# Kernel optimization log

Measured on AMD Instinct MI355X. Metric: run time of the kernel, lower is better.

## Reference

```python
import jax, jax.numpy as jnp
import numpy as np


def _conv1x1(w, x):
    # w: [out, in], x: [B, in, H, W] -> [B, out, H, W]
    return jnp.einsum('oc,bchw->bohw', w, x)


def _maxpool2(x):
    # 2x2 max pool, stride 2. x: [B, C, H, W] -> [B, C, H//2, W//2]
    B, C, H, W = x.shape
    return x.reshape(B, C, H // 2, 2, W // 2, 2).max(axis=(3, 5))


def setup_inputs() -> dict:
    key = jax.random.key(0)
    ks = jax.random.split(key, 5)
    B, C, H, W = 8, 256, 64, 64
    div = 8
    x = jax.random.normal(ks[0], (B, C, H, W), dtype=jnp.float32)
    wq = jax.random.normal(ks[1], (C // div, C), dtype=jnp.float32) * (C ** -0.5)
    wk = jax.random.normal(ks[2], (C // div, C), dtype=jnp.float32) * (C ** -0.5)
    wv = jax.random.normal(ks[3], (C // 2, C), dtype=jnp.float32) * (C ** -0.5)
    wo = jax.random.normal(ks[4], (C, C // 2), dtype=jnp.float32) * ((C // 2) ** -0.5)
    gamma = jnp.float32(0.5)  # nonzero so attention branch contributes
    return {"x": x, "wq": wq, "wk": wk, "wv": wv, "wo": wo, "gamma": gamma}


def reference(x, wq, wk, wv, wo, gamma):
    B, C, H, W = x.shape
    HW = H * W
    # query: [B, HW, Cq]
    q = _conv1x1(wq, x).reshape(B, -1, HW).transpose(0, 2, 1)
    # key: maxpool -> [B, Cq, HW//4]
    k = _maxpool2(_conv1x1(wk, x)).reshape(B, -1, HW // 4)
    # value: maxpool -> [B, C//2, HW//4]
    v = _maxpool2(_conv1x1(wv, x)).reshape(B, -1, HW // 4)
    scores = jnp.einsum('bnc,bcm->bnm', q, k)          # [B, HW, HW//4]
    attn = jax.nn.softmax(scores, axis=2)
    ctx = jnp.einsum('bcm,bnm->bcn', v, attn)          # [B, C//2, HW]
    ctx = ctx.reshape(B, C // 2, H, W)
    out = gamma * _conv1x1(wo, ctx) + x
    return out
```

## Files before the change

kernel.cpp:

```cpp
#include <hip/hip_runtime.h>
#include <hip/hip_bf16.h>

#define BB  8
#define CC  256
#define HW  4096
#define CQ  32
#define CV  128
#define MP  1024

#define XT_OFF  0
#define Y_OFF   4194304
#define KT_OFF  (Y_OFF + 3145728)
#define VP_OFF  (KT_OFF + 131072)
#define CT_OFF  (VP_OFF + 524288)
#define P0_OFF  CT_OFF
#define P1_OFF  XT_OFF
#define ML_OFF  (XT_OFF + 2097152)

typedef __attribute__((ext_vector_type(8))) short bf16x8;
typedef __attribute__((ext_vector_type(4))) short short4v;
typedef __attribute__((ext_vector_type(4))) float f32x4;

__device__ __forceinline__ short f2b(float f) {
    unsigned u = __float_as_uint(f);
    u += 0x7fffu + ((u >> 16) & 1u);
    return (short)(u >> 16);
}
__device__ __forceinline__ float b2f(short s) {
    return __uint_as_float(((unsigned)(unsigned short)s) << 16);
}

__global__ __launch_bounds__(256) void k_xt(
    const float* __restrict__ x, short* __restrict__ xt)
{
    __shared__ float t[64][65];
    const int bid = blockIdx.x;
    const int nt = bid & 63;
    const int ct = (bid >> 6) & 3;
    const int b  = bid >> 8;
    const int c0 = ct * 64, n0 = nt * 64;
    const int tid = threadIdx.x;

    const int col = tid & 63, wrow = (tid >> 6) * 16;
    #pragma unroll
    for (int i = 0; i < 16; ++i) {
        int r = wrow + i;
        t[r][col] = x[((long)(b * CC + c0 + r)) * HW + n0 + col];
    }
    __syncthreads();

    const int n = tid >> 2, cb = (tid & 3) * 16;
    short buf[16];
    #pragma unroll
    for (int j = 0; j < 16; ++j) buf[j] = f2b(t[cb + j][n]);
    short* dst = &xt[((long)(b * HW + n0 + n)) * CC + c0 + cb];
    *(int4*)dst = *(int4*)&buf[0];
    *(int4*)(dst + 8) = *(int4*)&buf[8];
}

__global__ __launch_bounds__(256) void k_qkv(
    const float* __restrict__ wq, const float* __restrict__ wk,
    const float* __restrict__ wv, const short* __restrict__ xt,
    short* __restrict__ y)
{
    __shared__ short w_lds[96 * 264];
    __shared__ short x_lds[256 * 40];
    const int bid = blockIdx.x;
    const int oc = bid & 1;
    const int nt = (bid >> 1) & 15;
    const int b  = bid >> 5;
    const int o0 = oc * 96, n0 = nt * 256;
    const int tid = threadIdx.x;
    const int lane = tid & 63;
    const int wvid = tid >> 6;
    const int l15 = lane & 15, g = lane >> 4;

    for (int it = 0; it < 24; ++it) {
        int idx = tid + it * 256;
        int ol = idx >> 6, cq = (idx & 63) * 4;
        int o = o0 + ol;
        const float* src = (o < 32) ? &wq[o * 256 + cq]
                         : (o < 64) ? &wk[(o - 32) * 256 + cq]
                                    : &wv[(o - 64) * 256 + cq];
        float4 w = *(const float4*)src;
        short4v p = { f2b(w.x), f2b(w.y), f2b(w.z), f2b(w.w) };
        *(short4v*)&w_lds[ol * 264 + cq] = p;
    }

    f32x4 acc[4][6];
    #pragma unroll
    for (int nf = 0; nf < 4; ++nf)
        #pragma unroll
        for (int of = 0; of < 6; ++of) acc[nf][of] = (f32x4){0.f, 0.f, 0.f, 0.f};

    for (int ks = 0; ks < 8; ++ks) {
        __syncthreads();
        {
            const short* src = &xt[((long)(b * HW + n0 + tid)) * CC + ks * 32];
            int4 v0 = *(const int4*)src;
            int4 v1 = *(const int4*)(src + 8);
            int4 v2 = *(const int4*)(src + 16);
            int4 v3 = *(const int4*)(src + 24);
            short* dst = &x_lds[tid * 40];
            *(int4*)dst = v0; *(int4*)(dst + 8) = v1;
            *(int4*)(dst + 16) = v2; *(int4*)(dst + 24) = v3;
        }
        __syncthreads();

        bf16x8 a[4], bf[6];
        #pragma unroll
        for (int nf = 0; nf < 4; ++nf)
            a[nf] = *(const bf16x8*)&x_lds[(wvid * 64 + nf * 16 + l15) * 40 + 8 * g];
        #pragma unroll
        for (int of = 0; of < 6; ++of)
            bf[of] = *(const bf16x8*)&w_lds[(of * 16 + l15) * 264 + ks * 32 + 8 * g];
        #pragma unroll
        for (int nf = 0; nf < 4; ++nf)
            #pragma unroll
            for (int of = 0; of < 6; ++of)
                acc[nf][of] = __builtin_amdgcn_mfma_f32_16x16x32_bf16(a[nf], bf[of], acc[nf][of], 0, 0, 0);
    }

    #pragma unroll
    for (int nf = 0; nf < 4; ++nf) {
        #pragma unroll
        for (int of = 0; of < 6; ++of) {
            int o = o0 + of * 16 + l15;
            long nb = (long)(b * HW + n0 + wvid * 64 + nf * 16 + 4 * g);
            #pragma unroll
            for (int r = 0; r < 4; ++r)
                y[(nb + r) * 192 + o] = f2b(acc[nf][of][r]);
        }
    }
}

__global__ __launch_bounds__(256) void k_pool(
    const short* __restrict__ y, short* __restrict__ kT, short* __restrict__ vp)
{
    __shared__ short t[64 * 136];
    const int bid = blockIdx.x;
    const int mt = bid & 15;
    const int b  = bid >> 4;
    const int m0 = mt * 64;
    const int tid = threadIdx.x;

    {
        int ml = tid >> 2, ci = (tid & 3) * 8;
        int pp = m0 + ml;
        int ph = pp >> 5, pw = pp & 31;
        const short* src = &y[((long)(b * HW) + ph * 128 + pw * 2) * 192 + 32 + ci];
        int4 s0 = *(const int4*)src;
        int4 s1 = *(const int4*)(src + 192);
        int4 s2 = *(const int4*)(src + 12288);
        int4 s3 = *(const int4*)(src + 12480);
        const short *a = (const short*)&s0, *bb = (const short*)&s1,
                    *c = (const short*)&s2, *d = (const short*)&s3;
        short o8[8];
        #pragma unroll
        for (int j = 0; j < 8; ++j)
            o8[j] = f2b(fmaxf(fmaxf(b2f(a[j]), b2f(bb[j])), fmaxf(b2f(c[j]), b2f(d[j]))));
        *(int4*)&kT[((long)(b * MP + pp)) * CQ + ci] = *(int4*)o8;
    }
    #pragma unroll
    for (int jj = 0; jj < 4; ++jj) {
        int idx = tid + jj * 256;
        int ml = idx >> 4, ci = (idx & 15) * 8;
        int pp = m0 + ml;
        int ph = pp >> 5, pw = pp & 31;
        const short* src = &y[((long)(b * HW) + ph * 128 + pw * 2) * 192 + 64 + ci];
        int4 s0 = *(const int4*)src;
        int4 s1 = *(const int4*)(src + 192);
        int4 s2 = *(const int4*)(src + 12288);
        int4 s3 = *(const int4*)(src + 12480);
        const short *a = (const short*)&s0, *bb = (const short*)&s1,
                    *c = (const short*)&s2, *d = (const short*)&s3;
        short o8[8];
        #pragma unroll
        for (int j = 0; j < 8; ++j)
            o8[j] = f2b(fmaxf(fmaxf(b2f(a[j]), b2f(bb[j])), fmaxf(b2f(c[j]), b2f(d[j]))));
        *(int4*)&t[ml * 136 + ci] = *(int4*)o8;
    }
    __syncthreads();
    {
        int c = tid & 127, mc = (tid >> 7) * 32;
        short buf[32];
        #pragma unroll
        for (int mm = 0; mm < 32; ++mm) buf[mm] = t[(mc + mm) * 136 + c];
        short* dst = &vp[((long)(b * CV + c)) * MP + m0 + mc];
        *(int4*)dst = *(int4*)&buf[0];
        *(int4*)(dst + 8)  = *(int4*)&buf[8];
        *(int4*)(dst + 16) = *(int4*)&buf[16];
        *(int4*)(dst + 24) = *(int4*)&buf[24];
    }
}

__global__ __launch_bounds__(128) void k_attn(
    const short* __restrict__ y,
    const short* __restrict__ kT,
    const short* __restrict__ vp,
    short* __restrict__ p0,
    short* __restrict__ p1,
    float* __restrict__ ml)
{
    __shared__ short p_lds[2][2][16][40];
    const int tid   = threadIdx.x;
    const int lane  = tid & 63;
    const int wid   = tid >> 6;
    const int split = blockIdx.x >> 9;
    const int rem   = blockIdx.x & 511;
    const int b     = rem >> 6;
    const int q0    = (rem & 63) * 64 + wid * 32;
    const int l15   = lane & 15;
    const int g     = lane >> 4;

    bf16x8 qf[2];
    const short* yq = y + (long)b * HW * 192;
    #pragma unroll
    for (int si = 0; si < 2; ++si)
        qf[si] = *(const bf16x8*)&yq[(long)(q0 + si * 16 + l15) * 192 + 8 * g];

    float m_run[2] = {-INFINITY, -INFINITY};
    float l_run[2] = {0.f, 0.f};
    f32x4 acc[2][8];
    #pragma unroll
    for (int si = 0; si < 2; ++si)
        #pragma unroll
        for (int ct = 0; ct < 8; ++ct)
            acc[si][ct] = (f32x4){0.f, 0.f, 0.f, 0.f};

    const short* kTb = kT + (long)b * MP * CQ;
    const short* vpb = vp + (long)b * CV * MP;

    for (int mt = 0; mt < 16; ++mt) {
        const int m0 = split * 512 + mt * 32;
        bf16x8 ka0 = *(const bf16x8*)&kTb[(m0 + l15) * CQ + 8 * g];
        bf16x8 ka1 = *(const bf16x8*)&kTb[(m0 + 16 + l15) * CQ + 8 * g];
        bf16x8 va[8];
        #pragma unroll
        for (int ct = 0; ct < 8; ++ct)
            va[ct] = *(const bf16x8*)&vpb[(ct * 16 + l15) * MP + m0 + 8 * g];

        #pragma unroll
        for (int si = 0; si < 2; ++si) {
            f32x4 s0 = (f32x4){0.f, 0.f, 0.f, 0.f};
            f32x4 s1 = (f32x4){0.f, 0.f, 0.f, 0.f};
            s0 = __builtin_amdgcn_mfma_f32_16x16x32_bf16(ka0, qf[si], s0, 0, 0, 0);
            s1 = __builtin_amdgcn_mfma_f32_16x16x32_bf16(ka1, qf[si], s1, 0, 0, 0);
            float tmax8 = fmaxf(fmaxf(fmaxf(s0[0], s0[1]), fmaxf(s0[2], s0[3])),
                                fmaxf(fmaxf(s1[0], s1[1]), fmaxf(s1[2], s1[3])));
            float mr = m_run[si];
            if (!__all(tmax8 <= mr + 8.0f)) {
                float tmax = fmaxf(tmax8, __shfl_xor(tmax8, 16, 64));
                tmax = fmaxf(tmax, __shfl_xor(tmax, 32, 64));
                float nm    = fmaxf(mr, tmax);
                float alpha = __expf(mr - nm);
                l_run[si] *= alpha;
                #pragma unroll
                for (int r = 0; r < 4; ++r) {
                    float ar = __shfl(alpha, 4 * g + r, 64);
                    #pragma unroll
                    for (int ct = 0; ct < 8; ++ct) acc[si][ct][r] *= ar;
                }
                m_run[si] = nm;
                mr = nm;
            }
            float p[8];
            #pragma unroll
            for (int r = 0; r < 4; ++r) { p[r] = __expf(s0[r] - mr); p[4 + r] = __expf(s1[r] - mr); }
            l_run[si] += ((p[0] + p[1]) + (p[2] + p[3])) + ((p[4] + p[5]) + (p[6] + p[7]));
            short4v w0 = { f2b(p[0]), f2b(p[1]), f2b(p[2]), f2b(p[3]) };
            short4v w1 = { f2b(p[4]), f2b(p[5]), f2b(p[6]), f2b(p[7]) };
            *(short4v*)&p_lds[wid][si][l15][4 * g]      = w0;
            *(short4v*)&p_lds[wid][si][l15][16 + 4 * g] = w1;
        }
        #pragma unroll
        for (int si = 0; si < 2; ++si) {
            bf16x8 pf = *(const bf16x8*)&p_lds[wid][si][l15][8 * g];
            #pragma unroll
            for (int ct = 0; ct < 8; ++ct)
                acc[si][ct] = __builtin_amdgcn_mfma_f32_16x16x32_bf16(pf, va[ct], acc[si][ct], 0, 0, 0);
        }
    }

    #pragma unroll
    for (int si = 0; si < 2; ++si) {
        l_run[si] += __shfl_xor(l_run[si], 16, 64);
        l_run[si] += __shfl_xor(l_run[si], 32, 64);
    }

    short* pp = split ? p1 : p0;
    #pragma unroll
    for (int si = 0; si < 2; ++si) {
        float inv = 1.f / l_run[si];
        #pragma unroll
        for (int r = 0; r < 4; ++r) {
            float invr = __shfl(inv, 4 * g + r, 64);
            long q = q0 + si * 16 + 4 * g + r;
            short* cb = &pp[((long)b * HW + q) * CV];
            #pragma unroll
            for (int ct = 0; ct < 8; ++ct)
                cb[ct * 16 + l15] = f2b(acc[si][ct][r] * invr);
        }
    }
    if (lane < 16) {
        #pragma unroll
        for (int si = 0; si < 2; ++si) {
            long row = (long)(split * BB + b) * HW + q0 + si * 16 + lane;
            ml[row * 2]     = m_run[si];
            ml[row * 2 + 1] = l_run[si];
        }
    }
}

__global__ __launch_bounds__(256) void k_out(
    const short* __restrict__ p0, const short* __restrict__ p1,
    const float* __restrict__ ml, const float* __restrict__ wo,
    const float* __restrict__ x, const float* __restrict__ gamma,
    float* __restrict__ out)
{
    __shared__ short c_lds[256 * 136];
    __shared__ short w_lds[128 * 136];
    const int bid = blockIdx.x;
    const int oc = bid & 1;
    const int nt = (bid >> 1) & 15;
    const int b  = bid >> 5;
    const int o0 = oc * 128, n0 = nt * 256;
    const int tid = threadIdx.x;
    const int lane = tid & 63;
    const int l15 = lane & 15, g = lane >> 4;
    const long NR = (long)BB * HW;

    {
        const long grow = (long)(b * HW + n0 + tid);
        const float m0v = ml[grow * 2],        l0v = ml[grow * 2 + 1];
        const float m1v = ml[(NR + grow) * 2], l1v = ml[(NR + grow) * 2 + 1];
        const float M = fmaxf(m0v, m1v);
        float w0 = l0v * __expf(m0v - M);
        float w1 = l1v * __expf(m1v - M);
        const float inv = 1.f / (w0 + w1);
        w0 *= inv; w1 *= inv;
        const short* s0 = &p0[grow * CV];
        const short* s1 = &p1[grow * CV];
        short* dst = &c_lds[tid * 136];
        #pragma unroll
        for (int j = 0; j < 16; ++j) {
            int4 a4 = *(const int4*)(s0 + 8 * j);
            int4 b4 = *(const int4*)(s1 + 8 * j);
            short o8[8];
            #pragma unroll
            for (int k = 0; k < 8; ++k)
                o8[k] = f2b(w0 * b2f(((const short*)&a4)[k])
                          + w1 * b2f(((const short*)&b4)[k]));
            *(int4*)(dst + 8 * j) = *(int4*)o8;
        }
    }
    for (int it = 0; it < 16; ++it) {
        int idx = tid + it * 256;
        int ol = idx >> 5, cq = (idx & 31) * 4;
        float4 w = *(const float4*)&wo[(o0 + ol) * CV + cq];
        short4v p = { f2b(w.x), f2b(w.y), f2b(w.z), f2b(w.w) };
        *(short4v*)&w_lds[ol * 136 + cq] = p;
    }
    __syncthreads();

    const int wvid = tid >> 6;
    const int ow = (wvid & 1) * 64, nw = (wvid >> 1) * 128;
    f32x4 acc[4][8];
    #pragma unroll
    for (int of = 0; of < 4; ++of)
        #pragma unroll
        for (int nf = 0; nf < 8; ++nf) acc[of][nf] = (f32x4){0.f, 0.f, 0.f, 0.f};

    #pragma unroll
    for (int ks = 0; ks < 4; ++ks) {
        bf16x8 af[4], bf[8];
        #pragma unroll
        for (int of = 0; of < 4; ++of)
            af[of] = *(const bf16x8*)&w_lds[(ow + of * 16 + l15) * 136 + ks * 32 + 8 * g];
        #pragma unroll
        for (int nf = 0; nf < 8; ++nf)
            bf[nf] = *(const bf16x8*)&c_lds[(nw + nf * 16 + l15) * 136 + ks * 32 + 8 * g];
        #pragma unroll
        for (int of = 0; of < 4; ++of)
            #pragma unroll
            for (int nf = 0; nf < 8; ++nf)
                acc[of][nf] = __builtin_amdgcn_mfma_f32_16x16x32_bf16(af[of], bf[nf], acc[of][nf], 0, 0, 0);
    }

    const float gma = gamma[0];
    #pragma unroll
    for (int of = 0; of < 4; ++of) {
        #pragma unroll
        for (int r = 0; r < 4; ++r) {
            int o = o0 + ow + of * 16 + 4 * g + r;
            #pragma unroll
            for (int nf = 0; nf < 8; ++nf) {
                int n = n0 + nw + nf * 16 + l15;
                long idx = (long)(b * CC + o) * HW + n;
                out[idx] = gma * acc[of][nf][r] + x[idx];
            }
        }
    }
}

extern "C" void kernel_launch(void* const* d_in, const int* in_sizes, int n_in,
                              void* d_out, int out_size, void* d_ws, size_t ws_size,
                              hipStream_t stream) {
    const float* x     = (const float*)d_in[0];
    const float* wq    = (const float*)d_in[1];
    const float* wk    = (const float*)d_in[2];
    const float* wv    = (const float*)d_in[3];
    const float* wo    = (const float*)d_in[4];
    const float* gamma = (const float*)d_in[5];
    float* out = (float*)d_out;
    float* ws  = (float*)d_ws;

    short* xt  = (short*)(ws + XT_OFF);
    short* y   = (short*)(ws + Y_OFF);
    short* kT  = (short*)(ws + KT_OFF);
    short* vp  = (short*)(ws + VP_OFF);
    short* p0  = (short*)(ws + P0_OFF);
    short* p1  = (short*)(ws + P1_OFF);
    float* mlb = ws + ML_OFF;

    k_xt  <<<dim3(2048), dim3(256), 0, stream>>>(x, xt);
    k_qkv <<<dim3(256),  dim3(256), 0, stream>>>(wq, wk, wv, xt, y);
    k_pool<<<dim3(128),  dim3(256), 0, stream>>>(y, kT, vp);
    k_attn<<<dim3(1024), dim3(128), 0, stream>>>(y, kT, vp, p0, p1, mlb);
    k_out <<<dim3(256),  dim3(256), 0, stream>>>(p0, p1, mlb, wo, x, gamma, out);
}
```

Baseline: 97.08 us.

## Software-pipeline attention loop so PV MFMAs overlap next tile's softmax

The flash-attention inner loop is restructured into a prologue, steady state and epilogue. Each iteration now issues the QK MFMAs for tile mt and the PV MFMAs for tile mt-1 before running the softmax for tile mt. This lets matrix-unit work overlap the exp and max VALU work and hides V-load latency by carrying V fragments across iterations. It costs extra registers for the carried V fragments and P values, which can lower occupancy or cause spills. The rescale of acc by alpha now happens after the previous tile's PV has been accumulated, which keeps the math consistent.

```diff
diff --git a/kernel.cpp b/kernel.cpp
--- a/kernel.cpp
+++ b/kernel.cpp
@@ -230,57 +230,91 @@
 
     const short* kTb = kT + (long)b * MP * CQ;
     const short* vpb = vp + (long)b * CV * MP;
-
-    for (int mt = 0; mt < 16; ++mt) {
-        const int m0 = split * 512 + mt * 32;
-        bf16x8 ka0 = *(const bf16x8*)&kTb[(m0 + l15) * CQ + 8 * g];
-        bf16x8 ka1 = *(const bf16x8*)&kTb[(m0 + 16 + l15) * CQ + 8 * g];
-        bf16x8 va[8];
+    const int mbase = split * 512;
+
+    auto softmax_step = [&](f32x4 sA, f32x4 sB, float& mrun, float& lrun,
+                            f32x4 (&accsi)[8], short (*plds)[40]) -> bf16x8 {
+        float tmax8 = fmaxf(fmaxf(fmaxf(sA[0], sA[1]), fmaxf(sA[2], sA[3])),
+                            fmaxf(fmaxf(sB[0], sB[1]), fmaxf(sB[2], sB[3])));
+        float mr = mrun;
+        if (!__all(tmax8 <= mr + 8.0f)) {
+            float tmax = fmaxf(tmax8, __shfl_xor(tmax8, 16, 64));
+            tmax = fmaxf(tmax, __shfl_xor(tmax, 32, 64));
+            float nm    = fmaxf(mr, tmax);
+            float alpha = __expf(mr - nm);
+            lrun *= alpha;
+            #pragma unroll
+            for (int r = 0; r < 4; ++r) {
+                float ar = __shfl(alpha, 4 * g + r, 64);
+                #pragma unroll
+                for (int ct = 0; ct < 8; ++ct) accsi[ct][r] *= ar;
+            }
+            mrun = nm;
+            mr = nm;
+        }
+        float p[8];
+        #pragma unroll
+        for (int r = 0; r < 4; ++r) { p[r] = __expf(sA[r] - mr); p[4 + r] = __expf(sB[r] - mr); }
+        lrun += ((p[0] + p[1]) + (p[2] + p[3])) + ((p[4] + p[5]) + (p[6] + p[7]));
+        short4v w0 = { f2b(p[0]), f2b(p[1]), f2b(p[2]), f2b(p[3]) };
+        short4v w1 = { f2b(p[4]), f2b(p[5]), f2b(p[6]), f2b(p[7]) };
+        *(short4v*)&plds[l15][4 * g]      = w0;
+        *(short4v*)&plds[l15][16 + 4 * g] = w1;
+        return *(const bf16x8*)&plds[l15][8 * g];
+    };
+
+    bf16x8 pfo0, pfo1, vao[8];
+    {
+        const int m0 = mbase;
+        bf16x8 kaA = *(const bf16x8*)&kTb[(m0 + l15) * CQ + 8 * g];
+        bf16x8 kaB = *(const bf16x8*)&kTb[(m0 + 16 + l15) * CQ + 8 * g];
         #pragma unroll
         for (int ct = 0; ct < 8; ++ct)
-            va[ct] = *(const bf16x8*)&vpb[(ct * 16 + l15) * MP + m0 + 8 * g];
-
-        #pragma unroll
-        for (int si = 0; si < 2; ++si) {
-            f32x4 s0 = (f32x4){0.f, 0.f, 0.f, 0.f};
-            f32x4 s1 = (f32x4){0.f, 0.f, 0.f, 0.f};
-            s0 = __builtin_amdgcn_mfma_f32_16x16x32_bf16(ka0, qf[si], s0, 0, 0, 0);
-            s1 = __builtin_amdgcn_mfma_f32_16x16x32_bf16(ka1, qf[si], s1, 0, 0, 0);
-            float tmax8 = fmaxf(fmaxf(fmaxf(s0[0], s0[1]), fmaxf(s0[2], s0[3])),
-                                fmaxf(fmaxf(s1[0], s1[1]), fmaxf(s1[2], s1[3])));
-            float mr = m_run[si];
-            if (!__all(tmax8 <= mr + 8.0f)) {
-                float tmax = fmaxf(tmax8, __shfl_xor(tmax8, 16, 64));
-                tmax = fmaxf(tmax, __shfl_xor(tmax, 32, 64));
-                float nm    = fmaxf(mr, tmax);
-                float alpha = __expf(mr - nm);
-                l_run[si] *= alpha;
-                #pragma unroll
-                for (int r = 0; r < 4; ++r) {
-                    float ar = __shfl(alpha, 4 * g + r, 64);
-                    #pragma unroll
-                    for (int ct = 0; ct < 8; ++ct) acc[si][ct][r] *= ar;
-                }
-                m_run[si] = nm;
-                mr = nm;
-            }
-            float p[8];
-            #pragma unroll
-            for (int r = 0; r < 4; ++r) { p[r] = __expf(s0[r] - mr); p[4 + r] = __expf(s1[r] - mr); }
-            l_run[si] += ((p[0] + p[1]) + (p[2] + p[3])) + ((p[4] + p[5]) + (p[6] + p[7]));
-            short4v w0 = { f2b(p[0]), f2b(p[1]), f2b(p[2]), f2b(p[3]) };
-            short4v w1 = { f2b(p[4]), f2b(p[5]), f2b(p[6]), f2b(p[7]) };
-            *(short4v*)&p_lds[wid][si][l15][4 * g]      = w0;
-            *(short4v*)&p_lds[wid][si][l15][16 + 4 * g] = w1;
-        }
-        #pragma unroll
-        for (int si = 0; si < 2; ++si) {
-            bf16x8 pf = *(const bf16x8*)&p_lds[wid][si][l15][8 * g];
-            #pragma unroll
-            for (int ct = 0; ct < 8; ++ct)
-                acc[si][ct] = __builtin_amdgcn_mfma_f32_16x16x32_bf16(pf, va[ct], acc[si][ct], 0, 0, 0);
-        }
-    }
+            vao[ct] = *(const bf16x8*)&vpb[(ct * 16 + l15) * MP + m0 + 8 * g];
+        f32x4 z = (f32x4){0.f, 0.f, 0.f, 0.f};
+        f32x4 t00 = __builtin_amdgcn_mfma_f32_16x16x32_bf16(kaA, qf[0], z, 0, 0, 0);
+        f32x4 t01 = __builtin_amdgcn_mfma_f32_16x16x32_bf16(kaB, qf[0], z, 0, 0, 0);
+        f32x4 t10 = __builtin_amdgcn_mfma_f32_16x16x32_bf16(kaA, qf[1], z, 0, 0, 0);
+        f32x4 t11 = __builtin_amdgcn_mfma_f32_16x16x32_bf16(kaB, qf[1], z, 0, 0, 0);
+        pfo0 = softmax_step(t00, t01, m_run[0], l_run[0], acc[0], p_lds[wid][0]);
+        pfo1 = softmax_step(t10, t11, m_run[1], l_run[1], acc[1], p_lds[wid][1]);
+    }
+
+    for (int mt = 1; mt < 16; ++mt) {
+        const int m0 = mbase + mt * 32;
+        bf16x8 kaA = *(const bf16x8*)&kTb[(m0 + l15) * CQ + 8 * g];
+        bf16x8 kaB = *(const bf16x8*)&kTb[(m0 + 16 + l15) * CQ + 8 * g];
+        bf16x8 van[8];
+        #pragma unroll
+        for (int ct = 0; ct < 8; ++ct)
+            van[ct] = *(const bf16x8*)&vpb[(ct * 16 + l15) * MP + m0 + 8 * g];
+
+        f32x4 z = (f32x4){0.f, 0.f, 0.f, 0.f};
+        f32x4 t00 = __builtin_amdgcn_mfma_f32_16x16x32_bf16(kaA, qf[0], z, 0, 0, 0);
+        f32x4 t01 = __builtin_amdgcn_mfma_f32_16x16x32_bf16(kaB, qf[0], z, 0, 0, 0);
+        f32x4 t10 = __builtin_amdgcn_mfma_f32_16x16x32_bf16(kaA, qf[1], z, 0, 0, 0);
+        f32x4 t11 = __builtin_amdgcn_mfma_f32_16x16x32_bf16(kaB, qf[1], z, 0, 0, 0);
+
+        #pragma unroll
+        for (int ct = 0; ct < 8; ++ct)
+            acc[0][ct] = __builtin_amdgcn_mfma_f32_16x16x32_bf16(pfo0, vao[ct], acc[0][ct], 0, 0, 0);
+        #pragma unroll
+        for (int ct = 0; ct < 8; ++ct)
+            acc[1][ct] = __builtin_amdgcn_mfma_f32_16x16x32_bf16(pfo1, vao[ct], acc[1][ct], 0, 0, 0);
+
+        pfo0 = softmax_step(t00, t01, m_run[0], l_run[0], acc[0], p_lds[wid][0]);
+        pfo1 = softmax_step(t10, t11, m_run[1], l_run[1], acc[1], p_lds[wid][1]);
+
+        #pragma unroll
+        for (int ct = 0; ct < 8; ++ct) vao[ct] = van[ct];
+    }
+
+    #pragma unroll
+    for (int ct = 0; ct < 8; ++ct)
+        acc[0][ct] = __builtin_amdgcn_mfma_f32_16x16x32_bf16(pfo0, vao[ct], acc[0][ct], 0, 0, 0);
+    #pragma unroll
+    for (int ct = 0; ct < 8; ++ct)
+        acc[1][ct] = __builtin_amdgcn_mfma_f32_16x16x32_bf16(pfo1, vao[ct], acc[1][ct], 0, 0, 0);
 
     #pragma unroll
     for (int si = 0; si < 2; ++si) {
```

Result: no change. 97.21 us (+0.1%).
